# Optimization experiments

Measured on AMD Instinct MI355X. Metric: run time of the kernel, lower is better.

## Reference

```python
import jax, jax.numpy as jnp
import numpy as np

N, D, R, C_IN = 384, 256, 64, 2
REL_H, NEI_H = 128, 256


def setup_inputs() -> dict:
    key = jax.random.key(0)
    ks = jax.random.split(key, 16)
    inp = {
        "corr_index": jax.random.normal(ks[0], (N, N, C_IN), jnp.float32),
        "nei_index": jax.random.randint(ks[1], (N, N), 0, 2, jnp.int32),
        "nei_num": jax.random.randint(ks[2], (N,), 0, N, jnp.int32),
        "outgate": jax.random.uniform(ks[3], (N, D), jnp.float32),
        "self_h": jax.random.normal(ks[4], (N, D), jnp.float32),
        "self_c": jax.random.normal(ks[5], (N, D), jnp.float32),
        # relativeLayer: 2-layer MLP, relu after both layers (iflastac=True)
        "rel_w1": jax.random.normal(ks[6], (C_IN, REL_H), jnp.float32) * 0.1,
        "rel_b1": jnp.zeros((REL_H,), jnp.float32),
        "rel_w2": jax.random.normal(ks[7], (REL_H, R), jnp.float32) * 0.1,
        "rel_b2": jnp.zeros((R,), jnp.float32),
        # ngate: single Linear(R+2D -> D) + sigmoid
        "ngate_w": jax.random.normal(ks[8], (R + 2 * D, D), jnp.float32) * 0.005,
        "ngate_b": jnp.zeros((D,), jnp.float32),
        # WAr: single Linear(R+2D -> 1), no activation (WAr_ac='')
        "war_w": jax.random.normal(ks[9], (R + 2 * D, 1), jnp.float32) * 0.05,
        "war_b": jnp.zeros((1,), jnp.float32),
        # W_nei: Linear(D->NEI_H)+relu, Linear(NEI_H->D), no last activation
        "wnei_w1": jax.random.normal(ks[10], (D, NEI_H), jnp.float32) * 0.05,
        "wnei_b1": jnp.zeros((NEI_H,), jnp.float32),
        "wnei_w2": jax.random.normal(ks[11], (NEI_H, D), jnp.float32) * 0.05,
        "wnei_b2": jnp.zeros((D,), jnp.float32),
    }
    return inp


def reference(corr_index, nei_index, nei_num, outgate, self_h, self_c,
              rel_w1, rel_b1, rel_w2, rel_b2, ngate_w, ngate_b,
              war_w, war_b, wnei_w1, wnei_b1, wnei_w2, wnei_b2):
    n, d = self_h.shape
    mask = nei_index > 0  # [N, N], pair (i, j)
    # relativeLayer on pairwise relative coords: relu(relu(x W1 + b1) W2 + b2)
    r = jax.nn.relu(jax.nn.relu(corr_index @ rel_w1 + rel_b1) @ rel_w2 + rel_b2)  # [N,N,R]
    # In torch code flat index k = i*N + j: hi_t[k] = self_h[i], nei_inputs[k] = self_h[j]
    h_i = jnp.broadcast_to(self_h[:, None, :], (n, n, d))
    h_j = jnp.broadcast_to(self_h[None, :, :], (n, n, d))
    feat = jnp.concatenate([r, h_i, h_j], axis=-1)  # [N,N,R+2D]
    gate = jax.nn.sigmoid(feat @ ngate_w + ngate_b)  # [N,N,D]
    msg = h_j * gate
    tt = (feat @ war_w + war_b)[..., 0]  # [N,N] attention logits
    # scatter into zero-init matrix, then Pos[Pos==0] = -inf, row softmax
    pos = jnp.where(mask, tt, 0.0)
    pos = jnp.where(pos == 0.0, -jnp.inf, pos)
    pos = jax.nn.softmax(pos, axis=1)  # [N,N]
    # masked, attention-weighted messages; guard NaN from fully-masked rows
    H = jnp.where(mask[:, :, None], msg * pos[:, :, None], 0.0)  # [N,N,D]
    h_sum = jnp.sum(H, axis=1)  # [N,D]
    h_sum = jax.nn.relu(h_sum @ wnei_w1 + wnei_b1) @ wnei_w2 + wnei_b2
    C = h_sum + self_c
    H_out = outgate * jnp.tanh(C)
    return (outgate, H_out, C)
```

## Files before the change

kernel.cpp:

```cpp
#include <hip/hip_runtime.h>
#include <hip/hip_bf16.h>
#include <math.h>

#define N 384
#define D 256
#define R 64
#define RELH 128
#define NN (N*N)
#define ND (N*D)
#define JCHUNK 64
#define NCHUNK (N / JCHUNK)
#define TPB 16
#define LOG2E 1.44269504088896f
#define HS_STRIDE 264

typedef _Float16 f16x8 __attribute__((ext_vector_type(8)));
typedef _Float16 f16x2 __attribute__((ext_vector_type(2)));
typedef float f32x4 __attribute__((ext_vector_type(4)));

__device__ __forceinline__ float fast_sigmoid(float x) {
    float e = __builtin_amdgcn_exp2f(-LOG2E * x);
    return __builtin_amdgcn_rcpf(1.f + e);
}
__device__ __forceinline__ float fast_exp(float x) {
    return __builtin_amdgcn_exp2f(LOG2E * x);
}
__device__ __forceinline__ float fast_tanh(float x) {
    float e = __builtin_amdgcn_exp2f(2.f * LOG2E * x);
    return 1.f - 2.f * __builtin_amdgcn_rcpf(1.f + e);
}

__global__ __launch_bounds__(256) void prep_kernel(
        const float* __restrict__ self_h, const float* __restrict__ ngate_w,
        const float* __restrict__ ngate_b, const float* __restrict__ war_w,
        const float* __restrict__ wnei_w1, const float* __restrict__ wnei_w2,
        const float* __restrict__ rel_w2,
        float* __restrict__ A, float* __restrict__ Bm,
        unsigned int* __restrict__ bh,
        float* __restrict__ u, float* __restrict__ v,
        _Float16* __restrict__ wf,
        _Float16* __restrict__ wf1, _Float16* __restrict__ wf2,
        _Float16* __restrict__ wfr) {
    int b = blockIdx.x, tid = threadIdx.x;
    int wv = tid >> 6, l = tid & 63;
    int lg = l >> 4, ln = l & 15;

    if (b < 6) {
        int r0 = b * 64 + wv * 16;
        for (int rr = 0; rr < 16; ++rr) {
            int row = r0 + rr;
            float su = 0.f, sv = 0.f;
            #pragma unroll
            for (int k = 0; k < 4; ++k) {
                int d = k * 64 + l;
                float h = self_h[row * D + d];
                su = fmaf(h, war_w[R + d], su);
                sv = fmaf(h, war_w[R + D + d], sv);
            }
            #pragma unroll
            for (int off = 32; off; off >>= 1) {
                su += __shfl_down(su, off);
                sv += __shfl_down(sv, off);
            }
            if (l == 0) { u[row] = su; v[row] = sv; }
        }
    } else if (b < 54) {
        int W = (b - 6) * 4 + wv;
        int m0 = (W >> 3) * 16;
        int cb = (W & 7) * 64;
        const float* wsrc = ngate_w + (size_t)(cb >= 256 ? 320 : 64) * D + (cb & 255);
        f32x4 acc[4];
        #pragma unroll
        for (int nt = 0; nt < 4; ++nt) acc[nt] = (f32x4){0.f, 0.f, 0.f, 0.f};
        #pragma unroll
        for (int s = 0; s < 8; ++s) {
            const float4* hp = (const float4*)&self_h[(size_t)(m0 + ln) * D + s * 32 + lg * 8];
            float4 h0 = hp[0], h1 = hp[1];
            f16x8 af;
            af[0] = (_Float16)h0.x; af[1] = (_Float16)h0.y;
            af[2] = (_Float16)h0.z; af[3] = (_Float16)h0.w;
            af[4] = (_Float16)h1.x; af[5] = (_Float16)h1.y;
            af[6] = (_Float16)h1.z; af[7] = (_Float16)h1.w;
            #pragma unroll
            for (int nt = 0; nt < 4; ++nt) {
                f16x8 bf;
                #pragma unroll
                for (int ii = 0; ii < 8; ++ii)
                    bf[ii] = (_Float16)wsrc[(size_t)(s * 32 + lg * 8 + ii) * D + nt * 16 + ln];
                acc[nt] = __builtin_amdgcn_mfma_f32_16x16x32_f16(af, bf, acc[nt], 0, 0, 0);
            }
        }
        #pragma unroll
        for (int nt = 0; nt < 4; ++nt)
            #pragma unroll
            for (int reg = 0; reg < 4; ++reg) {
                int row = m0 + lg * 4 + reg;
                int col = cb + nt * 16 + ln;
                if (col < 256) {
                    A[row * D + col] = acc[nt][reg] + ngate_b[col];
                } else {
                    int c2 = col - 256;
                    float bmv = acc[nt][reg];
                    Bm[row * D + c2] = bmv;
                    f16x2 pk;
                    pk[0] = (_Float16)bmv;
                    pk[1] = (_Float16)self_h[row * D + c2];
                    bh[row * D + c2] = __builtin_bit_cast(unsigned int, pk);
                }
            }
    } else if (b < 62) {
        int blkEq = (b - 54) * 4 + wv;
        int s = blkEq >> 4, t = blkEq & 15;
        #pragma unroll
        for (int ii = 0; ii < 8; ++ii) {
            float w = ngate_w[(s * 32 + lg * 8 + ii) * D + t * 16 + ln];
            wf[((size_t)(s * 16 + t) * 64 + l) * 8 + ii] = (_Float16)w;
        }
    } else if (b < 78) {
        int base = ((b - 62) * 4 + wv) * 4;
        #pragma unroll
        for (int k = 0; k < 4; ++k) {
            int T = base + k;
            int mat = T >> 7, rem = T & 127;
            int s = rem >> 4, t = rem & 15;
            const float* wsrc = mat ? wnei_w2 : wnei_w1;
            _Float16* dst = mat ? wf2 : wf1;
            #pragma unroll
            for (int ii = 0; ii < 8; ++ii) {
                float w = wsrc[(size_t)(s * 32 + lg * 8 + ii) * D + t * 16 + ln];
                dst[((size_t)(s * 16 + t) * 64 + l) * 8 + ii] = (_Float16)w;
            }
        }
    } else {
        #pragma unroll
        for (int k = 0; k < 4; ++k) {
            int T = wv * 4 + k;
            int s = T >> 2, nt = T & 3;
            #pragma unroll
            for (int ii = 0; ii < 8; ++ii) {
                float w = rel_w2[(size_t)(s * 32 + lg * 8 + ii) * R + nt * 16 + ln];
                wfr[((size_t)(s * 4 + nt) * 64 + l) * 8 + ii] = (_Float16)w;
            }
        }
    }
}

__global__ __launch_bounds__(256) void fused_kernel(
        const float* __restrict__ corr,
        const float* __restrict__ rel_w1, const float* __restrict__ rel_b1,
        const float* __restrict__ rel_b2,
        const float* __restrict__ war_w, const float* __restrict__ v,
        const int* __restrict__ nei,
        const _Float16* __restrict__ wfr, const _Float16* __restrict__ wf,
        const float* __restrict__ A, const unsigned int* __restrict__ bh,
        float* __restrict__ hsum) {
    __shared__ __align__(16) _Float16 rlds[N * R];
    __shared__ float ttrow[N];
    __shared__ float red[4];
    __shared__ float sM, sS;
    int i = blockIdx.x, tid = threadIdx.x;
    int wv = tid >> 6, l = tid & 63;
    int lg = l >> 4, ln = l & 15;
    char* rbase = (char*)rlds;

    float w10[4][8], w11[4][8], b1v[4][8];
    #pragma unroll
    for (int s = 0; s < 4; ++s)
        #pragma unroll
        for (int ii = 0; ii < 8; ++ii) {
            int hk = s * 32 + lg * 8 + ii;
            w10[s][ii] = rel_w1[hk];
            w11[s][ii] = rel_w1[RELH + hk];
            b1v[s][ii] = rel_b1[hk];
        }
    float b2r[4], warw[4];
    #pragma unroll
    for (int nt = 0; nt < 4; ++nt) {
        b2r[nt]  = rel_b2[nt * 16 + ln];
        warw[nt] = war_w[nt * 16 + ln];
    }

    #pragma unroll
    for (int t = 0; t < 6; ++t) {
        int j0 = (wv * 6 + t) * 16;
        float2 x = ((const float2*)corr)[(size_t)i * N + j0 + ln];
        f16x8 af[4];
        #pragma unroll
        for (int s = 0; s < 4; ++s)
            #pragma unroll
            for (int ii = 0; ii < 8; ++ii) {
                float h = fmaxf(0.f, fmaf(x.y, w11[s][ii], fmaf(x.x, w10[s][ii], b1v[s][ii])));
                af[s][ii] = (_Float16)h;
            }
        f32x4 c[4];
        #pragma unroll
        for (int nt = 0; nt < 4; ++nt) c[nt] = (f32x4){0.f, 0.f, 0.f, 0.f};
        #pragma unroll
        for (int nt = 0; nt < 4; ++nt)
            #pragma unroll
            for (int s = 0; s < 4; ++s) {
                f16x8 bfv = *(const f16x8*)&wfr[((size_t)(s * 4 + nt) * 64 + l) * 8];
                c[nt] = __builtin_amdgcn_mfma_f32_16x16x32_f16(af[s], bfv, c[nt], 0, 0, 0);
            }
        float tpart[4] = {0.f, 0.f, 0.f, 0.f};
        #pragma unroll
        for (int nt = 0; nt < 4; ++nt)
            #pragma unroll
            for (int reg = 0; reg < 4; ++reg) {
                float rv = fmaxf(0.f, c[nt][reg] + b2r[nt]);
                int j = j0 + lg * 4 + reg;
                int off = (j * 128 + (nt * 16 + ln) * 2) ^ ((j & 7) << 4);
                *(_Float16*)(rbase + off) = (_Float16)rv;
                tpart[reg] = fmaf(rv, warw[nt], tpart[reg]);
            }
        #pragma unroll
        for (int reg = 0; reg < 4; ++reg) {
            float tsum = tpart[reg];
            #pragma unroll
            for (int off = 8; off; off >>= 1) tsum += __shfl_xor(tsum, off, 16);
            tpart[reg] = tsum;
        }
        if (ln == 0) {
            #pragma unroll
            for (int reg = 0; reg < 4; ++reg) {
                int j = j0 + lg * 4 + reg;
                ttrow[j] = tpart[reg] + v[j];
            }
        }
    }
    __syncthreads();

    {
        float tv1 = ttrow[tid];
        bool va1 = (nei[(size_t)i * N + tid] > 0) && (tv1 != 0.f);
        float tv2 = 0.f; bool va2 = false;
        if (tid < N - 256) {
            tv2 = ttrow[tid + 256];
            va2 = (nei[(size_t)i * N + tid + 256] > 0) && (tv2 != 0.f);
        }
        float m = va1 ? tv1 : -INFINITY;
        if (va2) m = fmaxf(m, tv2);
        #pragma unroll
        for (int off = 32; off; off >>= 1) m = fmaxf(m, __shfl_down(m, off));
        if (l == 0) red[wv] = m;
        __syncthreads();
        if (tid == 0) sM = fmaxf(fmaxf(red[0], red[1]), fmaxf(red[2], red[3]));
        __syncthreads();
        float M = sM;
        float e1 = 0.f, e2 = 0.f;
        if (M != -INFINITY) {
            if (va1) e1 = fast_exp(tv1 - M);
            if (va2) e2 = fast_exp(tv2 - M);
        }
        float sum = e1 + e2;
        #pragma unroll
        for (int off = 32; off; off >>= 1) sum += __shfl_down(sum, off);
        if (l == 0) red[wv] = sum;
        __syncthreads();
        if (tid == 0) sS = red[0] + red[1] + red[2] + red[3];
        __syncthreads();
        float rden = (sS > 0.f) ? __builtin_amdgcn_rcpf(sS) : 0.f;
        ttrow[tid] = va1 ? e1 * rden : 0.f;
        if (tid < N - 256) ttrow[tid + 256] = va2 ? e2 * rden : 0.f;
    }
    __syncthreads();

    f16x8 bf[2][4];
    #pragma unroll
    for (int s = 0; s < 2; ++s)
        #pragma unroll
        for (int dt = 0; dt < 4; ++dt)
            bf[s][dt] = *(const f16x8*)&wf[((size_t)(s * 16 + wv * 4 + dt) * 64 + l) * 8];
    float based[4];
    #pragma unroll
    for (int dt = 0; dt < 4; ++dt)
        based[dt] = A[i * D + wv * 64 + dt * 16 + ln];

    float acc[4] = {0.f, 0.f, 0.f, 0.f};
    for (int jt = 0; jt < 24; ++jt) {
        int jb = jt * 16;
        f16x8 afr[2];
        #pragma unroll
        for (int s = 0; s < 2; ++s) {
            int j = jb + ln;
            int off = (j * 128 + (s * 64 + lg * 16)) ^ ((j & 7) << 4);
            afr[s] = *(const f16x8*)(rbase + off);
        }
        f32x4 c[4];
        #pragma unroll
        for (int dt = 0; dt < 4; ++dt) c[dt] = (f32x4){0.f, 0.f, 0.f, 0.f};
        #pragma unroll
        for (int dt = 0; dt < 4; ++dt)
            #pragma unroll
            for (int s = 0; s < 2; ++s)
                c[dt] = __builtin_amdgcn_mfma_f32_16x16x32_f16(afr[s], bf[s][dt], c[dt], 0, 0, 0);
        #pragma unroll
        for (int reg = 0; reg < 4; ++reg) {
            int jj = jb + lg * 4 + reg;
            float p = ttrow[jj];
            #pragma unroll
            for (int dt = 0; dt < 4; ++dt) {
                int d = wv * 64 + dt * 16 + ln;
                unsigned int uu = bh[(size_t)jj * D + d];
                f16x2 bhv = __builtin_bit_cast(f16x2, uu);
                float logit = c[dt][reg] + based[dt] + (float)bhv[0];
                float g = fast_sigmoid(logit);
                acc[dt] = fmaf(p * g, (float)bhv[1], acc[dt]);
            }
        }
    }
    #pragma unroll
    for (int dt = 0; dt < 4; ++dt) {
        float a = acc[dt];
        a += __shfl_xor(a, 16);
        a += __shfl_xor(a, 32);
        acc[dt] = a;
    }
    if (lg == 0) {
        #pragma unroll
        for (int dt = 0; dt < 4; ++dt)
            hsum[(size_t)i * D + wv * 64 + dt * 16 + ln] = acc[dt];
    }
}

__global__ __launch_bounds__(256) void tt_valu_kernel(
        const float* __restrict__ corr,
        const float* __restrict__ rel_w1, const float* __restrict__ rel_b1,
        const float* __restrict__ rel_w2, const float* __restrict__ rel_b2,
        const float* __restrict__ war_w, const float* __restrict__ war_b,
        const float* __restrict__ u, const float* __restrict__ v,
        float* __restrict__ tt) {
    __shared__ __align__(16) float h1s[4][RELH];
    int tid = threadIdx.x, w = tid >> 6, l = tid & 63;
    float w1a0 = rel_w1[l],      w1a1 = rel_w1[RELH + l];
    float w1b0 = rel_w1[64 + l], w1b1 = rel_w1[RELH + 64 + l];
    float b1a = rel_b1[l], b1b = rel_b1[64 + l];
    float b2v = rel_b2[l], warw = war_w[l], wb = war_b[0];
    int pbase = blockIdx.x * TPB;
    #pragma unroll
    for (int it = 0; it < TPB / 4; ++it) {
        int p = pbase + it * 4 + w;
        int i = p / N, j = p - i * N;
        float2 x = *(const float2*)(corr + p * 2);
        h1s[w][l]      = fmaxf(0.f, fmaf(x.y, w1a1, fmaf(x.x, w1a0, b1a)));
        h1s[w][l + 64] = fmaxf(0.f, fmaf(x.y, w1b1, fmaf(x.x, w1b0, b1b)));
        float c0 = b2v, c1 = 0.f, c2 = 0.f, c3 = 0.f;
        const float4* hv = (const float4*)h1s[w];
        #pragma unroll
        for (int k4 = 0; k4 < RELH / 4; ++k4) {
            float4 h = hv[k4];
            c0 = fmaf(h.x, rel_w2[(k4 * 4 + 0) * R + l], c0);
            c1 = fmaf(h.y, rel_w2[(k4 * 4 + 1) * R + l], c1);
            c2 = fmaf(h.z, rel_w2[(k4 * 4 + 2) * R + l], c2);
            c3 = fmaf(h.w, rel_w2[(k4 * 4 + 3) * R + l], c3);
// ... 85 lines not shown
                c1 = fmaf(h.y, rel_w2[(k + 1) * R + l], c1);
                c2 = fmaf(h.z, rel_w2[(k + 2) * R + l], c2);
                c3 = fmaf(h.w, rel_w2[(k + 3) * R + l], c3);
            }
            rs[w][l] = fmaxf(0.f, (c0 + c1) + (c2 + c3));
        }
        __syncthreads();
        #pragma unroll
        for (int ww = 0; ww < 4; ++ww) {
            float wtj = wsh[ww];
            if (wtj != 0.f) {
                int jj = j0 + ww;
                const float4* rv = (const float4*)rs[ww];
                float l0 = 0.f, l1 = 0.f, l2 = 0.f, l3 = 0.f;
                #pragma unroll 4
                for (int m4 = 0; m4 < R / 4; ++m4) {
                    float4 r4 = rv[m4];
                    int m = m4 * 4;
                    l0 = fmaf(r4.x, ngate_w[m * D + tid], l0);
                    l1 = fmaf(r4.y, ngate_w[(m + 1) * D + tid], l1);
                    l2 = fmaf(r4.z, ngate_w[(m + 2) * D + tid], l2);
                    l3 = fmaf(r4.w, ngate_w[(m + 3) * D + tid], l3);
                }
                float logit = base + Bm[jj * D + tid] + ((l0 + l1) + (l2 + l3));
                float g = fast_sigmoid(logit);
                acc = fmaf(wtj * self_h[jj * D + tid], g, acc);
            }
        }
        __syncthreads();
    }
    partial[(blockIdx.y * N + i) * D + tid] = acc;
}

template<int CHUNKS>
__global__ __launch_bounds__(256, 2) void final_mfma_kernel(
        const float* __restrict__ partial,
        const _Float16* __restrict__ wf1, const _Float16* __restrict__ wf2,
        const float* __restrict__ wnei_b1, const float* __restrict__ wnei_b2,
        const float* __restrict__ self_c, const float* __restrict__ outgate,
        float* __restrict__ out) {
    __shared__ _Float16 hs16[16][HS_STRIDE];
    __shared__ _Float16 hid16[16][HS_STRIDE];
    int i0 = blockIdx.x * 16;
    int tid = threadIdx.x, wv = tid >> 6, l = tid & 63;
    int lg = l >> 4, ln = l & 15;

    #pragma unroll
    for (int s = 0; s < 4; ++s) {
        int f4 = tid + s * 256;
        int row = f4 >> 6, c4 = f4 & 63;
        float4 a = {0.f, 0.f, 0.f, 0.f};
        #pragma unroll
        for (int c = 0; c < CHUNKS; ++c) {
            float4 p = ((const float4*)partial)[(size_t)(c * N + i0 + row) * (D / 4) + c4];
            a.x += p.x; a.y += p.y; a.z += p.z; a.w += p.w;
        }
        hs16[row][c4 * 4 + 0] = (_Float16)a.x;
        hs16[row][c4 * 4 + 1] = (_Float16)a.y;
        hs16[row][c4 * 4 + 2] = (_Float16)a.z;
        hs16[row][c4 * 4 + 3] = (_Float16)a.w;
    }
    __syncthreads();

    {
        f32x4 c1[4];
        #pragma unroll
// ... 49 lines not shown
    }
}

extern "C" void kernel_launch(void* const* d_in, const int* in_sizes, int n_in,
                              void* d_out, int out_size, void* d_ws, size_t ws_size,
                              hipStream_t stream) {
    const float* corr    = (const float*)d_in[0];
    const int*   nei     = (const int*)d_in[1];
    const float* outg    = (const float*)d_in[3];
    const float* self_h  = (const float*)d_in[4];
    const float* self_c  = (const float*)d_in[5];
    const float* rel_w1  = (const float*)d_in[6];
    const float* rel_b1  = (const float*)d_in[7];
    const float* rel_w2  = (const float*)d_in[8];
    const float* rel_b2  = (const float*)d_in[9];
    const float* ngate_w = (const float*)d_in[10];
    const float* ngate_b = (const float*)d_in[11];
    const float* war_w   = (const float*)d_in[12];
    const float* war_b   = (const float*)d_in[13];
    const float* wnei_w1 = (const float*)d_in[14];
    const float* wnei_b1 = (const float*)d_in[15];
    const float* wnei_w2 = (const float*)d_in[16];
    const float* wnei_b2 = (const float*)d_in[17];

    float* ws      = (float*)d_ws;
    float* tt      = ws;
    float* pos     = ws + NN;
    float* A       = ws + 2 * NN;
    float* Bm      = ws + 2 * NN + ND;
    float* u       = ws + 2 * NN + 2 * ND;
    float* v       = u + N;
    float* partial = v + N;
    unsigned int* bh = (unsigned int*)(partial + NCHUNK * ND);
    float* tail    = (float*)(bh + ND);
    _Float16* wf   = (_Float16*)tail;
    _Float16* wf1  = wf + 2 * 16 * 64 * 8;
    _Float16* wf2  = wf1 + 8 * 16 * 64 * 8;
    _Float16* wfr  = wf2 + 8 * 16 * 64 * 8;
    size_t base_floats = (size_t)(2 * NN + 3 * ND + 2 * N + NCHUNK * ND);
    size_t f16_count = (size_t)(2 + 8 + 8) * 16 * 64 * 8 + 16 * 64 * 8;
    size_t need = (base_floats + f16_count / 2 + 16) * sizeof(float);
    bool use_fused = ws_size >= need;
    float* out = (float*)d_out;

    prep_kernel<<<79, 256, 0, stream>>>(self_h, ngate_w, ngate_b, war_w,
                                        wnei_w1, wnei_w2, rel_w2,
                                        A, Bm, bh, u, v, wf, wf1, wf2, wfr);
    if (use_fused) {
        fused_kernel<<<N, 256, 0, stream>>>(corr, rel_w1, rel_b1, rel_b2,
                                            war_w, v, nei, wfr, wf, A, bh, partial);
        final_mfma_kernel<1><<<N / 16, 256, 0, stream>>>(partial, wf1, wf2,
                                                         wnei_b1, wnei_b2,
                                                         self_c, outg, out);
    } else {
        tt_valu_kernel<<<NN / TPB, 256, 0, stream>>>(corr, rel_w1, rel_b1, rel_w2, rel_b2,
                                                     war_w, war_b, u, v, tt);
        softmax_kernel<<<N, 256, 0, stream>>>(tt, nei, pos);
        dim3 ggrid(N, NCHUNK);
        gate_norc_kernel<<<ggrid, 256, 0, stream>>>(corr, rel_w1, rel_b1, rel_w2, rel_b2,
                                                    ngate_w, A, Bm, pos, self_h,
                                                    partial);
        final_mfma_kernel<NCHUNK><<<N / 16, 256, 0, stream>>>(partial, wf1, wf2,
                                                              wnei_b1, wnei_b2,
                                                              self_c, outg, out);
    }
}
```

Measured before the change: 58.37 us.

## Split fused kernel over two j-halves per row and prefetch bh values

Launches the fused kernel on a 2D grid so each row i gets two blocks, each handling half of the neighbour columns for the gated message accumulation. The per-half results are written as partial sums that the final kernel reduces (template parameter now 2). LDS for the relative features is halved, which should allow more resident blocks. Each block still recomputes the full relative MLP and logits for the whole row so the softmax stays exact, so that stage's work is duplicated. It also hoists the bh loads ahead of the MFMA in each tile to hide their latency.

After: 66.52 us. 14.0% more time.

```diff
diff --git a/kernel.cpp b/kernel.cpp
--- a/kernel.cpp
+++ b/kernel.cpp
@@ -13,6 +13,7 @@
 #define TPB 16
 #define LOG2E 1.44269504088896f
 #define HS_STRIDE 264
+#define JH 192
 
 typedef _Float16 f16x8 __attribute__((ext_vector_type(8)));
 typedef _Float16 f16x2 __attribute__((ext_vector_type(2)));
@@ -153,78 +154,86 @@
         const int* __restrict__ nei,
         const _Float16* __restrict__ wfr, const _Float16* __restrict__ wf,
         const float* __restrict__ A, const unsigned int* __restrict__ bh,
-        float* __restrict__ hsum) {
-    __shared__ __align__(16) _Float16 rlds[N * R];
+        float* __restrict__ partial) {
+    __shared__ __align__(16) _Float16 rlds[JH * R];
     __shared__ float ttrow[N];
     __shared__ float red[4];
     __shared__ float sM, sS;
-    int i = blockIdx.x, tid = threadIdx.x;
+    int i = blockIdx.x, jhalf = blockIdx.y;
+    int jbase = jhalf * JH;
+    int tid = threadIdx.x;
     int wv = tid >> 6, l = tid & 63;
     int lg = l >> 4, ln = l & 15;
     char* rbase = (char*)rlds;
 
-    float w10[4][8], w11[4][8], b1v[4][8];
-    #pragma unroll
-    for (int s = 0; s < 4; ++s)
-        #pragma unroll
-        for (int ii = 0; ii < 8; ++ii) {
-            int hk = s * 32 + lg * 8 + ii;
-            w10[s][ii] = rel_w1[hk];
-            w11[s][ii] = rel_w1[RELH + hk];
-            b1v[s][ii] = rel_b1[hk];
-        }
-    float b2r[4], warw[4];
-    #pragma unroll
-    for (int nt = 0; nt < 4; ++nt) {
-        b2r[nt]  = rel_b2[nt * 16 + ln];
-        warw[nt] = war_w[nt * 16 + ln];
-    }
-
-    #pragma unroll
-    for (int t = 0; t < 6; ++t) {
-        int j0 = (wv * 6 + t) * 16;
-        float2 x = ((const float2*)corr)[(size_t)i * N + j0 + ln];
-        f16x8 af[4];
+    {
+        float w10[4][8], w11[4][8], b1v[4][8];
         #pragma unroll
         for (int s = 0; s < 4; ++s)
             #pragma unroll
             for (int ii = 0; ii < 8; ++ii) {
-                float h = fmaxf(0.f, fmaf(x.y, w11[s][ii], fmaf(x.x, w10[s][ii], b1v[s][ii])));
-                af[s][ii] = (_Float16)h;
-            }
-        f32x4 c[4];
-        #pragma unroll
-        for (int nt = 0; nt < 4; ++nt) c[nt] = (f32x4){0.f, 0.f, 0.f, 0.f};
-        #pragma unroll
-        for (int nt = 0; nt < 4; ++nt)
-            #pragma unroll
-            for (int s = 0; s < 4; ++s) {
-                f16x8 bfv = *(const f16x8*)&wfr[((size_t)(s * 4 + nt) * 64 + l) * 8];
-                c[nt] = __builtin_amdgcn_mfma_f32_16x16x32_f16(af[s], bfv, c[nt], 0, 0, 0);
-            }
-        float tpart[4] = {0.f, 0.f, 0.f, 0.f};
-        #pragma unroll
-        for (int nt = 0; nt < 4; ++nt)
+                int hk = s * 32 + lg * 8 + ii;
+                w10[s][ii] = rel_w1[hk];
+                w11[s][ii] = rel_w1[RELH + hk];
+                b1v[s][ii] = rel_b1[hk];
+            }
+        float b2r[4], warw[4];
+        #pragma unroll
+        for (int nt = 0; nt < 4; ++nt) {
+            b2r[nt]  = rel_b2[nt * 16 + ln];
+            warw[nt] = war_w[nt * 16 + ln];
+        }
+
+        #pragma unroll
+        for (int t = 0; t < 6; ++t) {
+            int tile = wv * 6 + t;
+            int j0 = tile * 16;
+            bool mine = (j0 >= jbase) && (j0 < jbase + JH);
+            float2 x = ((const float2*)corr)[(size_t)i * N + j0 + ln];
+            f16x8 af[4];
+            #pragma unroll
+            for (int s = 0; s < 4; ++s)
+                #pragma unroll
+                for (int ii = 0; ii < 8; ++ii) {
+                    float h = fmaxf(0.f, fmaf(x.y, w11[s][ii], fmaf(x.x, w10[s][ii], b1v[s][ii])));
+                    af[s][ii] = (_Float16)h;
+                }
+            f32x4 c[4];
+            #pragma unroll
+            for (int nt = 0; nt < 4; ++nt) c[nt] = (f32x4){0.f, 0.f, 0.f, 0.f};
+            #pragma unroll
+            for (int nt = 0; nt < 4; ++nt)
+                #pragma unroll
+                for (int s = 0; s < 4; ++s) {
+                    f16x8 bfv = *(const f16x8*)&wfr[((size_t)(s * 4 + nt) * 64 + l) * 8];
+                    c[nt] = __builtin_amdgcn_mfma_f32_16x16x32_f16(af[s], bfv, c[nt], 0, 0, 0);
+                }
+            float tpart[4] = {0.f, 0.f, 0.f, 0.f};
+            #pragma unroll
+            for (int nt = 0; nt < 4; ++nt)
+                #pragma unroll
+                for (int reg = 0; reg < 4; ++reg) {
+                    float rv = fmaxf(0.f, c[nt][reg] + b2r[nt]);
+                    if (mine) {
+                        int lj = j0 - jbase + lg * 4 + reg;
+                        int off = (lj * 128 + (nt * 16 + ln) * 2) ^ ((lj & 7) << 4);
+                        *(_Float16*)(rbase + off) = (_Float16)rv;
+                    }
+                    tpart[reg] = fmaf(rv, warw[nt], tpart[reg]);
+                }
             #pragma unroll
             for (int reg = 0; reg < 4; ++reg) {
-                float rv = fmaxf(0.f, c[nt][reg] + b2r[nt]);
-                int j = j0 + lg * 4 + reg;
-                int off = (j * 128 + (nt * 16 + ln) * 2) ^ ((j & 7) << 4);
-                *(_Float16*)(rbase + off) = (_Float16)rv;
-                tpart[reg] = fmaf(rv, warw[nt], tpart[reg]);
-            }
-        #pragma unroll
-        for (int reg = 0; reg < 4; ++reg) {
-            float tsum = tpart[reg];
-            #pragma unroll
-            for (int off = 8; off; off >>= 1) tsum += __shfl_xor(tsum, off, 16);
-            tpart[reg] = tsum;
-        }
-        if (ln == 0) {
-            #pragma unroll
-            for (int reg = 0; reg < 4; ++reg) {
-                int j = j0 + lg * 4 + reg;
-                ttrow[j] = tpart[reg] + v[j];
+                float tsum = tpart[reg];
+                #pragma unroll
+                for (int off = 8; off; off >>= 1) tsum += __shfl_xor(tsum, off, 16);
+                tpart[reg] = tsum;
+            }
+            if (ln == 0) {
+                #pragma unroll
+                for (int reg = 0; reg < 4; ++reg) {
+                    int j = j0 + lg * 4 + reg;
+                    ttrow[j] = tpart[reg] + v[j];
+                }
             }
         }
     }
@@ -277,13 +286,21 @@
         based[dt] = A[i * D + wv * 64 + dt * 16 + ln];
 
     float acc[4] = {0.f, 0.f, 0.f, 0.f};
-    for (int jt = 0; jt < 24; ++jt) {
-        int jb = jt * 16;
+    for (int jt = 0; jt < JH / 16; ++jt) {
+        int ljb = jt * 16;
+        unsigned int uu[4][4];
+        #pragma unroll
+        for (int reg = 0; reg < 4; ++reg) {
+            int jj = jbase + ljb + lg * 4 + reg;
+            #pragma unroll
+            for (int dt = 0; dt < 4; ++dt)
+                uu[reg][dt] = bh[(size_t)jj * D + wv * 64 + dt * 16 + ln];
+        }
         f16x8 afr[2];
         #pragma unroll
         for (int s = 0; s < 2; ++s) {
-            int j = jb + ln;
-            int off = (j * 128 + (s * 64 + lg * 16)) ^ ((j & 7) << 4);
+            int lj = ljb + ln;
+            int off = (lj * 128 + (s * 64 + lg * 16)) ^ ((lj & 7) << 4);
             afr[s] = *(const f16x8*)(rbase + off);
         }
         f32x4 c[4];
@@ -296,13 +313,11 @@
                 c[dt] = __builtin_amdgcn_mfma_f32_16x16x32_f16(afr[s], bf[s][dt], c[dt], 0, 0, 0);
         #pragma unroll
         for (int reg = 0; reg < 4; ++reg) {
-            int jj = jb + lg * 4 + reg;
+            int jj = jbase + ljb + lg * 4 + reg;
             float p = ttrow[jj];
             #pragma unroll
             for (int dt = 0; dt < 4; ++dt) {
-                int d = wv * 64 + dt * 16 + ln;
-                unsigned int uu = bh[(size_t)jj * D + d];
-                f16x2 bhv = __builtin_bit_cast(f16x2, uu);
+                f16x2 bhv = __builtin_bit_cast(f16x2, uu[reg][dt]);
                 float logit = c[dt][reg] + based[dt] + (float)bhv[0];
                 float g = fast_sigmoid(logit);
                 acc[dt] = fmaf(p * g, (float)bhv[1], acc[dt]);
@@ -319,7 +334,7 @@
     if (lg == 0) {
         #pragma unroll
         for (int dt = 0; dt < 4; ++dt)
-            hsum[(size_t)i * D + wv * 64 + dt * 16 + ln] = acc[dt];
+            partial[(size_t)(jhalf * N + i) * D + wv * 64 + dt * 16 + ln] = acc[dt];
     }
 }
 
@@ -601,9 +616,10 @@
                                         wnei_w1, wnei_w2, rel_w2,
                                         A, Bm, bh, u, v, wf, wf1, wf2, wfr);
     if (use_fused) {
-        fused_kernel<<<N, 256, 0, stream>>>(corr, rel_w1, rel_b1, rel_b2,
-                                            war_w, v, nei, wfr, wf, A, bh, partial);
-        final_mfma_kernel<1><<<N / 16, 256, 0, stream>>>(partial, wf1, wf2,
+        dim3 fgrid(N, 2);
+        fused_kernel<<<fgrid, 256, 0, stream>>>(corr, rel_w1, rel_b1, rel_b2,
+                                                war_w, v, nei, wfr, wf, A, bh, partial);
+        final_mfma_kernel<2><<<N / 16, 256, 0, stream>>>(partial, wf1, wf2,
                                                          wnei_b1, wnei_b2,
                                                          self_c, outg, out);
     } else {
```

## Prefetch gate operands, fold log2e into weights, pack layer-1 MLP in f16

Applied to the files above, without the earlier changes.

The gate loop in the fused kernel now double-buffers the bh global loads one tile ahead and seeds the MFMA accumulators with the per-row bias. The -log2e factor is folded into the prepared f16 ngate weights and the bh values, so the sigmoid becomes a bare exp2 plus reciprocal. The first relative-MLP layer is computed with packed f16x2 arithmetic instead of scalar fp32. The prep kernel is split into more, smaller tiles by raising its block count from 79 to 127. The goal is to hide global-load latency and cut VALU work. The cost is higher register pressure and lower precision in the first layer, which now runs in f16.

After: 66.09 us. 1.13x slower.

```diff
diff --git a/kernel.cpp b/kernel.cpp
--- a/kernel.cpp
+++ b/kernel.cpp
@@ -17,6 +17,8 @@
 typedef _Float16 f16x8 __attribute__((ext_vector_type(8)));
 typedef _Float16 f16x2 __attribute__((ext_vector_type(2)));
 typedef float f32x4 __attribute__((ext_vector_type(4)));
+
+union F16U8 { f16x8 v8; f16x2 p2[4]; };
 
 __device__ __forceinline__ float fast_sigmoid(float x) {
     float e = __builtin_amdgcn_exp2f(-LOG2E * x);
@@ -64,14 +66,14 @@
             }
             if (l == 0) { u[row] = su; v[row] = sv; }
         }
-    } else if (b < 54) {
+    } else if (b < 102) {
         int W = (b - 6) * 4 + wv;
-        int m0 = (W >> 3) * 16;
-        int cb = (W & 7) * 64;
+        int m0 = (W >> 4) * 16;
+        int cb = (W & 15) * 32;
         const float* wsrc = ngate_w + (size_t)(cb >= 256 ? 320 : 64) * D + (cb & 255);
-        f32x4 acc[4];
-        #pragma unroll
-        for (int nt = 0; nt < 4; ++nt) acc[nt] = (f32x4){0.f, 0.f, 0.f, 0.f};
+        f32x4 acc[2];
+        #pragma unroll
+        for (int nt = 0; nt < 2; ++nt) acc[nt] = (f32x4){0.f, 0.f, 0.f, 0.f};
         #pragma unroll
         for (int s = 0; s < 8; ++s) {
             const float4* hp = (const float4*)&self_h[(size_t)(m0 + ln) * D + s * 32 + lg * 8];
@@ -82,16 +84,16 @@
             af[4] = (_Float16)h1.x; af[5] = (_Float16)h1.y;
             af[6] = (_Float16)h1.z; af[7] = (_Float16)h1.w;
             #pragma unroll
-            for (int nt = 0; nt < 4; ++nt) {
+            for (int nt = 0; nt < 2; ++nt) {
                 f16x8 bf;
                 #pragma unroll
                 for (int ii = 0; ii < 8; ++ii)
-                    bf[ii] = (_Float16)wsrc[(size_t)(s * 32 + lg * 8 + ii) * D + nt * 16 + ln];
+                    bf[ii] = (_Float16)wsrc[(size_t)(s * 32 + lg * 8 + ii) * D + ((cb & 31) + nt * 16 + ln)];
                 acc[nt] = __builtin_amdgcn_mfma_f32_16x16x32_f16(af, bf, acc[nt], 0, 0, 0);
             }
         }
         #pragma unroll
-        for (int nt = 0; nt < 4; ++nt)
+        for (int nt = 0; nt < 2; ++nt)
             #pragma unroll
             for (int reg = 0; reg < 4; ++reg) {
                 int row = m0 + lg * 4 + reg;
@@ -103,21 +105,21 @@
                     float bmv = acc[nt][reg];
                     Bm[row * D + c2] = bmv;
                     f16x2 pk;
-                    pk[0] = (_Float16)bmv;
+                    pk[0] = (_Float16)(bmv * (-LOG2E));
                     pk[1] = (_Float16)self_h[row * D + c2];
                     bh[row * D + c2] = __builtin_bit_cast(unsigned int, pk);
                 }
             }
-    } else if (b < 62) {
-        int blkEq = (b - 54) * 4 + wv;
+    } else if (b < 110) {
+        int blkEq = (b - 102) * 4 + wv;
         int s = blkEq >> 4, t = blkEq & 15;
         #pragma unroll
         for (int ii = 0; ii < 8; ++ii) {
             float w = ngate_w[(s * 32 + lg * 8 + ii) * D + t * 16 + ln];
-            wf[((size_t)(s * 16 + t) * 64 + l) * 8 + ii] = (_Float16)w;
-        }
-    } else if (b < 78) {
-        int base = ((b - 62) * 4 + wv) * 4;
+            wf[((size_t)(s * 16 + t) * 64 + l) * 8 + ii] = (_Float16)(w * (-LOG2E));
+        }
+    } else if (b < 126) {
+        int base = ((b - 110) * 4 + wv) * 4;
         #pragma unroll
         for (int k = 0; k < 4; ++k) {
             int T = base + k;
@@ -163,68 +165,73 @@
     int lg = l >> 4, ln = l & 15;
     char* rbase = (char*)rlds;
 
-    float w10[4][8], w11[4][8], b1v[4][8];
-    #pragma unroll
-    for (int s = 0; s < 4; ++s)
-        #pragma unroll
-        for (int ii = 0; ii < 8; ++ii) {
-            int hk = s * 32 + lg * 8 + ii;
-            w10[s][ii] = rel_w1[hk];
-            w11[s][ii] = rel_w1[RELH + hk];
-            b1v[s][ii] = rel_b1[hk];
-        }
-    float b2r[4], warw[4];
-    #pragma unroll
-    for (int nt = 0; nt < 4; ++nt) {
-        b2r[nt]  = rel_b2[nt * 16 + ln];
-        warw[nt] = war_w[nt * 16 + ln];
-    }
-
-    #pragma unroll
-    for (int t = 0; t < 6; ++t) {
-        int j0 = (wv * 6 + t) * 16;
-        float2 x = ((const float2*)corr)[(size_t)i * N + j0 + ln];
-        f16x8 af[4];
+    {
+        f16x2 w10p[4][4], w11p[4][4], b1p[4][4];
         #pragma unroll
         for (int s = 0; s < 4; ++s)
             #pragma unroll
-            for (int ii = 0; ii < 8; ++ii) {
-                float h = fmaxf(0.f, fmaf(x.y, w11[s][ii], fmaf(x.x, w10[s][ii], b1v[s][ii])));
-                af[s][ii] = (_Float16)h;
-            }
-        f32x4 c[4];
-        #pragma unroll
-        for (int nt = 0; nt < 4; ++nt) c[nt] = (f32x4){0.f, 0.f, 0.f, 0.f};
-        #pragma unroll
-        for (int nt = 0; nt < 4; ++nt)
-            #pragma unroll
-            for (int s = 0; s < 4; ++s) {
-                f16x8 bfv = *(const f16x8*)&wfr[((size_t)(s * 4 + nt) * 64 + l) * 8];
-                c[nt] = __builtin_amdgcn_mfma_f32_16x16x32_f16(af[s], bfv, c[nt], 0, 0, 0);
-            }
-        float tpart[4] = {0.f, 0.f, 0.f, 0.f};
-        #pragma unroll
-        for (int nt = 0; nt < 4; ++nt)
+            for (int q = 0; q < 4; ++q) {
+                int hk = s * 32 + lg * 8 + q * 2;
+                w10p[s][q] = (f16x2){(_Float16)rel_w1[hk], (_Float16)rel_w1[hk + 1]};
+                w11p[s][q] = (f16x2){(_Float16)rel_w1[RELH + hk], (_Float16)rel_w1[RELH + hk + 1]};
+                b1p[s][q]  = (f16x2){(_Float16)rel_b1[hk], (_Float16)rel_b1[hk + 1]};
+            }
+        float b2r[4], warw[4];
+        #pragma unroll
+        for (int nt = 0; nt < 4; ++nt) {
+            b2r[nt]  = rel_b2[nt * 16 + ln];
+            warw[nt] = war_w[nt * 16 + ln];
+        }
+
+        #pragma unroll
+        for (int t = 0; t < 6; ++t) {
+            int j0 = (wv * 6 + t) * 16;
+            float2 x = ((const float2*)corr)[(size_t)i * N + j0 + ln];
+            _Float16 xh0 = (_Float16)x.x, xh1 = (_Float16)x.y;
+            f16x2 x0p = {xh0, xh0}, x1p = {xh1, xh1};
+            f16x2 zero2 = {(_Float16)0.f, (_Float16)0.f};
+            F16U8 af[4];
+            #pragma unroll
+            for (int s = 0; s < 4; ++s)
+                #pragma unroll
+                for (int q = 0; q < 4; ++q) {
+                    f16x2 hp = x0p * w10p[s][q] + (x1p * w11p[s][q] + b1p[s][q]);
+                    af[s].p2[q] = __builtin_elementwise_max(hp, zero2);
+                }
+            f32x4 c[4];
+            #pragma unroll
+            for (int nt = 0; nt < 4; ++nt) c[nt] = (f32x4){0.f, 0.f, 0.f, 0.f};
+            #pragma unroll
+            for (int nt = 0; nt < 4; ++nt)
+                #pragma unroll
+                for (int s = 0; s < 4; ++s) {
+                    f16x8 bfv = *(const f16x8*)&wfr[((size_t)(s * 4 + nt) * 64 + l) * 8];
+                    c[nt] = __builtin_amdgcn_mfma_f32_16x16x32_f16(af[s].v8, bfv, c[nt], 0, 0, 0);
+                }
+            float tpart[4] = {0.f, 0.f, 0.f, 0.f};
+            #pragma unroll
+            for (int nt = 0; nt < 4; ++nt)
+                #pragma unroll
+                for (int reg = 0; reg < 4; ++reg) {
+                    float rv = fmaxf(0.f, c[nt][reg] + b2r[nt]);
+                    int j = j0 + lg * 4 + reg;
+                    int off = (j * 128 + (nt * 16 + ln) * 2) ^ ((j & 7) << 4);
+                    *(_Float16*)(rbase + off) = (_Float16)rv;
+                    tpart[reg] = fmaf(rv, warw[nt], tpart[reg]);
+                }
             #pragma unroll
             for (int reg = 0; reg < 4; ++reg) {
-                float rv = fmaxf(0.f, c[nt][reg] + b2r[nt]);
-                int j = j0 + lg * 4 + reg;
-                int off = (j * 128 + (nt * 16 + ln) * 2) ^ ((j & 7) << 4);
-                *(_Float16*)(rbase + off) = (_Float16)rv;
-                tpart[reg] = fmaf(rv, warw[nt], tpart[reg]);
-            }
-        #pragma unroll
-        for (int reg = 0; reg < 4; ++reg) {
-            float tsum = tpart[reg];
-            #pragma unroll
-            for (int off = 8; off; off >>= 1) tsum += __shfl_xor(tsum, off, 16);
-            tpart[reg] = tsum;
-        }
-        if (ln == 0) {
-            #pragma unroll
-            for (int reg = 0; reg < 4; ++reg) {
-                int j = j0 + lg * 4 + reg;
-                ttrow[j] = tpart[reg] + v[j];
+                float tsum = tpart[reg];
+                #pragma unroll
+                for (int off = 8; off; off >>= 1) tsum += __shfl_xor(tsum, off, 16);
+                tpart[reg] = tsum;
+            }
+            if (ln == 0) {
+                #pragma unroll
+                for (int reg = 0; reg < 4; ++reg) {
+                    int j = j0 + lg * 4 + reg;
+                    ttrow[j] = tpart[reg] + v[j];
+                }
             }
         }
     }
@@ -274,41 +281,66 @@
     float based[4];
     #pragma unroll
     for (int dt = 0; dt < 4; ++dt)
-        based[dt] = A[i * D + wv * 64 + dt * 16 + ln];
+        based[dt] = (-LOG2E) * A[i * D + wv * 64 + dt * 16 + ln];
 
     float acc[4] = {0.f, 0.f, 0.f, 0.f};
-    for (int jt = 0; jt < 24; ++jt) {
-        int jb = jt * 16;
-        f16x8 afr[2];
-        #pragma unroll
-        for (int s = 0; s < 2; ++s) {
-            int j = jb + ln;
-            int off = (j * 128 + (s * 64 + lg * 16)) ^ ((j & 7) << 4);
-            afr[s] = *(const f16x8*)(rbase + off);
-        }
-        f32x4 c[4];
-        #pragma unroll
-        for (int dt = 0; dt < 4; ++dt) c[dt] = (f32x4){0.f, 0.f, 0.f, 0.f};
-        #pragma unroll
-        for (int dt = 0; dt < 4; ++dt)
-            #pragma unroll
-            for (int s = 0; s < 2; ++s)
-                c[dt] = __builtin_amdgcn_mfma_f32_16x16x32_f16(afr[s], bf[s][dt], c[dt], 0, 0, 0);
-        #pragma unroll
-        for (int reg = 0; reg < 4; ++reg) {
-            int jj = jb + lg * 4 + reg;
-            float p = ttrow[jj];
-            #pragma unroll
-            for (int dt = 0; dt < 4; ++dt) {
-                int d = wv * 64 + dt * 16 + ln;
-                unsigned int uu = bh[(size_t)jj * D + d];
-                f16x2 bhv = __builtin_bit_cast(f16x2, uu);
-                float logit = c[dt][reg] + based[dt] + (float)bhv[0];
-                float g = fast_sigmoid(logit);
-                acc[dt] = fmaf(p * g, (float)bhv[1], acc[dt]);
-            }
-        }
-    }
+
+    unsigned int uuA[4][4], uuB[4][4];
+    #define LOAD_UU(buf, jtv)                                                   \
+        {                                                                       \
+            int jb_ = (jtv) * 16;                                               \
+            _Pragma("unroll")                                                   \
+            for (int reg = 0; reg < 4; ++reg) {                                 \
+                int jj_ = jb_ + lg * 4 + reg;                                   \
+                _Pragma("unroll")                                               \
+                for (int dt = 0; dt < 4; ++dt)                                  \
+                    buf[reg][dt] = bh[(size_t)jj_ * D + wv * 64 + dt * 16 + ln];\
+            }                                                                   \
+        }
+    #define GATE_STEP(jtv, buf)                                                 \
+        {                                                                       \
+            int ljb_ = (jtv) * 16;                                              \
+            f16x8 afr[2];                                                       \
+            _Pragma("unroll")                                                   \
+            for (int s = 0; s < 2; ++s) {                                       \
+                int lj_ = ljb_ + ln;                                            \
+                int off_ = (lj_ * 128 + (s * 64 + lg * 16)) ^ ((lj_ & 7) << 4); \
+                afr[s] = *(const f16x8*)(rbase + off_);                         \
+            }                                                                   \
+            f32x4 c[4];                                                         \
+            _Pragma("unroll")                                                   \
+            for (int dt = 0; dt < 4; ++dt)                                      \
+                c[dt] = (f32x4){based[dt], based[dt], based[dt], based[dt]};    \
+            _Pragma("unroll")                                                   \
+            for (int dt = 0; dt < 4; ++dt)                                      \
+                _Pragma("unroll")                                               \
+                for (int s = 0; s < 2; ++s)                                     \
+                    c[dt] = __builtin_amdgcn_mfma_f32_16x16x32_f16(afr[s], bf[s][dt], c[dt], 0, 0, 0); \
+            _Pragma("unroll")                                                   \
+            for (int reg = 0; reg < 4; ++reg) {                                 \
+                int jj_ = ljb_ + lg * 4 + reg;                                  \
+                float p_ = ttrow[jj_];                                          \
+                _Pragma("unroll")                                               \
+                for (int dt = 0; dt < 4; ++dt) {                                \
+                    f16x2 bhv = __builtin_bit_cast(f16x2, buf[reg][dt]);        \
+                    float slog = c[dt][reg] + (float)bhv[0];                    \
+                    float g_ = __builtin_amdgcn_rcpf(1.f + __builtin_amdgcn_exp2f(slog)); \
+                    acc[dt] = fmaf(p_ * g_, (float)bhv[1], acc[dt]);            \
+                }                                                               \
+            }                                                                   \
+        }
+
+    LOAD_UU(uuA, 0);
+    #pragma unroll 2
+    for (int jt2 = 0; jt2 < 12; ++jt2) {
+        LOAD_UU(uuB, 2 * jt2 + 1);
+        GATE_STEP(2 * jt2, uuA);
+        if (jt2 < 11) LOAD_UU(uuA, 2 * jt2 + 2);
+        GATE_STEP(2 * jt2 + 1, uuB);
+    }
+    #undef LOAD_UU
+    #undef GATE_STEP
+
     #pragma unroll
     for (int dt = 0; dt < 4; ++dt) {
         float a = acc[dt];
@@ -597,9 +629,9 @@
     bool use_fused = ws_size >= need;
     float* out = (float*)d_out;
 
-    prep_kernel<<<79, 256, 0, stream>>>(self_h, ngate_w, ngate_b, war_w,
-                                        wnei_w1, wnei_w2, rel_w2,
-                                        A, Bm, bh, u, v, wf, wf1, wf2, wfr);
+    prep_kernel<<<127, 256, 0, stream>>>(self_h, ngate_w, ngate_b, war_w,
+                                         wnei_w1, wnei_w2, rel_w2,
+                                         A, Bm, bh, u, v, wf, wf1, wf2, wfr);
     if (use_fused) {
         fused_kernel<<<N, 256, 0, stream>>>(corr, rel_w1, rel_b1, rel_b2,
                                             war_w, v, nei, wfr, wf, A, bh, partial);
```

## Split fused kernel over j into three chunks with flash-style softmax merge

Applied to the files above, without the earlier changes.

The fused per-row kernel now runs on a 2D grid that splits the j dimension into three chunks, so there are three times as many blocks, each with a smaller LDS footprint. Each chunk computes a local max and sum of exponentials and writes them alongside unnormalised partial sums. A new final kernel rescales and combines the partials with online-softmax weights before the W_nei MLP. The aim is better occupancy and SM fill on a chip with many CUs, at the cost of extra partial traffic and a merge step. Chunks where 128 j values leave only two 16-row tiles per wave may give low per-block work.

After: 59.50 us. No clear change (+1.9%).

```diff
diff --git a/kernel.cpp b/kernel.cpp
--- a/kernel.cpp
+++ b/kernel.cpp
@@ -13,6 +13,8 @@
 #define TPB 16
 #define LOG2E 1.44269504088896f
 #define HS_STRIDE 264
+#define SPLIT 3
+#define JS (N / SPLIT)
 
 typedef _Float16 f16x8 __attribute__((ext_vector_type(8)));
 typedef _Float16 f16x2 __attribute__((ext_vector_type(2)));
@@ -153,93 +155,94 @@
         const int* __restrict__ nei,
         const _Float16* __restrict__ wfr, const _Float16* __restrict__ wf,
         const float* __restrict__ A, const unsigned int* __restrict__ bh,
-        float* __restrict__ hsum) {
-    __shared__ __align__(16) _Float16 rlds[N * R];
-    __shared__ float ttrow[N];
+        float* __restrict__ partial,
+        float* __restrict__ mbuf, float* __restrict__ sbuf) {
+    __shared__ __align__(16) _Float16 rlds[JS * R];
+    __shared__ float ttrow[JS];
     __shared__ float red[4];
     __shared__ float sM, sS;
-    int i = blockIdx.x, tid = threadIdx.x;
+    int i = blockIdx.x, chunk = blockIdx.y;
+    int jbase = chunk * JS;
+    int tid = threadIdx.x;
     int wv = tid >> 6, l = tid & 63;
     int lg = l >> 4, ln = l & 15;
     char* rbase = (char*)rlds;
 
-    float w10[4][8], w11[4][8], b1v[4][8];
-    #pragma unroll
-    for (int s = 0; s < 4; ++s)
-        #pragma unroll
-        for (int ii = 0; ii < 8; ++ii) {
-            int hk = s * 32 + lg * 8 + ii;
-            w10[s][ii] = rel_w1[hk];
-            w11[s][ii] = rel_w1[RELH + hk];
-            b1v[s][ii] = rel_b1[hk];
-        }
-    float b2r[4], warw[4];
-    #pragma unroll
-    for (int nt = 0; nt < 4; ++nt) {
-        b2r[nt]  = rel_b2[nt * 16 + ln];
-        warw[nt] = war_w[nt * 16 + ln];
-    }
-
-    #pragma unroll
-    for (int t = 0; t < 6; ++t) {
-        int j0 = (wv * 6 + t) * 16;
-        float2 x = ((const float2*)corr)[(size_t)i * N + j0 + ln];
-        f16x8 af[4];
+    {
+        float w10[4][8], w11[4][8], b1v[4][8];
         #pragma unroll
         for (int s = 0; s < 4; ++s)
             #pragma unroll
             for (int ii = 0; ii < 8; ++ii) {
-                float h = fmaxf(0.f, fmaf(x.y, w11[s][ii], fmaf(x.x, w10[s][ii], b1v[s][ii])));
-                af[s][ii] = (_Float16)h;
-            }
-        f32x4 c[4];
-        #pragma unroll
-        for (int nt = 0; nt < 4; ++nt) c[nt] = (f32x4){0.f, 0.f, 0.f, 0.f};
-        #pragma unroll
-        for (int nt = 0; nt < 4; ++nt)
-            #pragma unroll
-            for (int s = 0; s < 4; ++s) {
-                f16x8 bfv = *(const f16x8*)&wfr[((size_t)(s * 4 + nt) * 64 + l) * 8];
-                c[nt] = __builtin_amdgcn_mfma_f32_16x16x32_f16(af[s], bfv, c[nt], 0, 0, 0);
-            }
-        float tpart[4] = {0.f, 0.f, 0.f, 0.f};
-        #pragma unroll
-        for (int nt = 0; nt < 4; ++nt)
+                int hk = s * 32 + lg * 8 + ii;
+                w10[s][ii] = rel_w1[hk];
+                w11[s][ii] = rel_w1[RELH + hk];
+                b1v[s][ii] = rel_b1[hk];
+            }
+        float b2r[4], warw[4];
+        #pragma unroll
+        for (int nt = 0; nt < 4; ++nt) {
+            b2r[nt]  = rel_b2[nt * 16 + ln];
+            warw[nt] = war_w[nt * 16 + ln];
+        }
+
+        #pragma unroll
+        for (int t = 0; t < 2; ++t) {
+            int lj0 = (wv * 2 + t) * 16;
+            int jg0 = jbase + lj0;
+            float2 x = ((const float2*)corr)[(size_t)i * N + jg0 + ln];
+            f16x8 af[4];
+            #pragma unroll
+            for (int s = 0; s < 4; ++s)
+                #pragma unroll
+                for (int ii = 0; ii < 8; ++ii) {
+                    float h = fmaxf(0.f, fmaf(x.y, w11[s][ii], fmaf(x.x, w10[s][ii], b1v[s][ii])));
+                    af[s][ii] = (_Float16)h;
+                }
+            f32x4 c[4];
+            #pragma unroll
+            for (int nt = 0; nt < 4; ++nt) c[nt] = (f32x4){0.f, 0.f, 0.f, 0.f};
+            #pragma unroll
+            for (int nt = 0; nt < 4; ++nt)
+                #pragma unroll
+                for (int s = 0; s < 4; ++s) {
+                    f16x8 bfv = *(const f16x8*)&wfr[((size_t)(s * 4 + nt) * 64 + l) * 8];
+                    c[nt] = __builtin_amdgcn_mfma_f32_16x16x32_f16(af[s], bfv, c[nt], 0, 0, 0);
+                }
+            float tpart[4] = {0.f, 0.f, 0.f, 0.f};
+            #pragma unroll
+            for (int nt = 0; nt < 4; ++nt)
+                #pragma unroll
+                for (int reg = 0; reg < 4; ++reg) {
+                    float rv = fmaxf(0.f, c[nt][reg] + b2r[nt]);
+                    int lj = lj0 + lg * 4 + reg;
+                    int off = (lj * 128 + (nt * 16 + ln) * 2) ^ ((lj & 7) << 4);
+                    *(_Float16*)(rbase + off) = (_Float16)rv;
+                    tpart[reg] = fmaf(rv, warw[nt], tpart[reg]);
+                }
             #pragma unroll
             for (int reg = 0; reg < 4; ++reg) {
-                float rv = fmaxf(0.f, c[nt][reg] + b2r[nt]);
-                int j = j0 + lg * 4 + reg;
-                int off = (j * 128 + (nt * 16 + ln) * 2) ^ ((j & 7) << 4);
-                *(_Float16*)(rbase + off) = (_Float16)rv;
-                tpart[reg] = fmaf(rv, warw[nt], tpart[reg]);
-            }
-        #pragma unroll
-        for (int reg = 0; reg < 4; ++reg) {
-            float tsum = tpart[reg];
-            #pragma unroll
-            for (int off = 8; off; off >>= 1) tsum += __shfl_xor(tsum, off, 16);
-            tpart[reg] = tsum;
-        }
-        if (ln == 0) {
-            #pragma unroll
-            for (int reg = 0; reg < 4; ++reg) {
-                int j = j0 + lg * 4 + reg;
-                ttrow[j] = tpart[reg] + v[j];
+                float tsum = tpart[reg];
+                #pragma unroll
+                for (int off = 8; off; off >>= 1) tsum += __shfl_xor(tsum, off, 16);
+                tpart[reg] = tsum;
+            }
+            if (ln == 0) {
+                #pragma unroll
+                for (int reg = 0; reg < 4; ++reg) {
+                    int lj = lj0 + lg * 4 + reg;
+                    ttrow[lj] = tpart[reg] + v[jbase + lj];
+                }
             }
         }
     }
     __syncthreads();
 
     {
-        float tv1 = ttrow[tid];
-        bool va1 = (nei[(size_t)i * N + tid] > 0) && (tv1 != 0.f);
-        float tv2 = 0.f; bool va2 = false;
-        if (tid < N - 256) {
-            tv2 = ttrow[tid + 256];
-            va2 = (nei[(size_t)i * N + tid + 256] > 0) && (tv2 != 0.f);
-        }
-        float m = va1 ? tv1 : -INFINITY;
-        if (va2) m = fmaxf(m, tv2);
+        bool act = tid < JS;
+        float tv = act ? ttrow[tid] : 0.f;
+        bool va = act && (nei[(size_t)i * N + jbase + tid] > 0) && (tv != 0.f);
+        float m = va ? tv : -INFINITY;
         #pragma unroll
         for (int off = 32; off; off >>= 1) m = fmaxf(m, __shfl_down(m, off));
         if (l == 0) red[wv] = m;
@@ -247,21 +250,21 @@
         if (tid == 0) sM = fmaxf(fmaxf(red[0], red[1]), fmaxf(red[2], red[3]));
         __syncthreads();
         float M = sM;
-        float e1 = 0.f, e2 = 0.f;
-        if (M != -INFINITY) {
-            if (va1) e1 = fast_exp(tv1 - M);
-            if (va2) e2 = fast_exp(tv2 - M);
-        }
-        float sum = e1 + e2;
+        float e = 0.f;
+        if (va && M != -INFINITY) e = fast_exp(tv - M);
+        float sum = e;
         #pragma unroll
         for (int off = 32; off; off >>= 1) sum += __shfl_down(sum, off);
         if (l == 0) red[wv] = sum;
         __syncthreads();
-        if (tid == 0) sS = red[0] + red[1] + red[2] + red[3];
+        if (tid == 0) {
+            float ss = red[0] + red[1] + red[2] + red[3];
+            sS = ss;
+            mbuf[chunk * N + i] = M;
+            sbuf[chunk * N + i] = ss;
+        }
         __syncthreads();
-        float rden = (sS > 0.f) ? __builtin_amdgcn_rcpf(sS) : 0.f;
-        ttrow[tid] = va1 ? e1 * rden : 0.f;
-        if (tid < N - 256) ttrow[tid + 256] = va2 ? e2 * rden : 0.f;
+        if (act) ttrow[tid] = e;
     }
     __syncthreads();
 
@@ -277,13 +280,13 @@
         based[dt] = A[i * D + wv * 64 + dt * 16 + ln];
 
     float acc[4] = {0.f, 0.f, 0.f, 0.f};
-    for (int jt = 0; jt < 24; ++jt) {
+    for (int jt = 0; jt < JS / 16; ++jt) {
         int jb = jt * 16;
         f16x8 afr[2];
         #pragma unroll
         for (int s = 0; s < 2; ++s) {
-            int j = jb + ln;
-            int off = (j * 128 + (s * 64 + lg * 16)) ^ ((j & 7) << 4);
+            int lj = jb + ln;
+            int off = (lj * 128 + (s * 64 + lg * 16)) ^ ((lj & 7) << 4);
             afr[s] = *(const f16x8*)(rbase + off);
         }
         f32x4 c[4];
@@ -296,8 +299,9 @@
                 c[dt] = __builtin_amdgcn_mfma_f32_16x16x32_f16(afr[s], bf[s][dt], c[dt], 0, 0, 0);
         #pragma unroll
         for (int reg = 0; reg < 4; ++reg) {
-            int jj = jb + lg * 4 + reg;
-            float p = ttrow[jj];
+            int lj = jb + lg * 4 + reg;
+            float p = ttrow[lj];
+            int jj = jbase + lj;
             #pragma unroll
             for (int dt = 0; dt < 4; ++dt) {
                 int d = wv * 64 + dt * 16 + ln;
@@ -319,7 +323,7 @@
     if (lg == 0) {
         #pragma unroll
         for (int dt = 0; dt < 4; ++dt)
-            hsum[(size_t)i * D + wv * 64 + dt * 16 + ln] = acc[dt];
+            partial[(size_t)(chunk * N + i) * D + wv * 64 + dt * 16 + ln] = acc[dt];
     }
 }
 
@@ -471,6 +475,117 @@
     partial[(blockIdx.y * N + i) * D + tid] = acc;
 }
 
+__global__ __launch_bounds__(256, 2) void final_w_kernel(
+        const float* __restrict__ partial,
+        const float* __restrict__ mbuf, const float* __restrict__ sbuf,
+        const _Float16* __restrict__ wf1, const _Float16* __restrict__ wf2,
+        const float* __restrict__ wnei_b1, const float* __restrict__ wnei_b2,
+        const float* __restrict__ self_c, const float* __restrict__ outgate,
+        float* __restrict__ out) {
+    __shared__ _Float16 hs16[16][HS_STRIDE];
+    __shared__ _Float16 hid16[16][HS_STRIDE];
+    __shared__ float alpha[16][SPLIT];
+    int i0 = blockIdx.x * 16;
+    int tid = threadIdx.x, wv = tid >> 6, l = tid & 63;
+    int lg = l >> 4, ln = l & 15;
+
+    if (tid < 16) {
+        int row = i0 + tid;
+        float mv[SPLIT];
+        float M = -INFINITY;
+        #pragma unroll
+        for (int c = 0; c < SPLIT; ++c) {
+            mv[c] = mbuf[c * N + row];
+            M = fmaxf(M, mv[c]);
+        }
+        float a[SPLIT];
+        float S = 0.f;
+        #pragma unroll
+        for (int c = 0; c < SPLIT; ++c) {
+            float t = (mv[c] == -INFINITY) ? 0.f : fast_exp(mv[c] - M);
+            a[c] = t;
+            S = fmaf(t, sbuf[c * N + row], S);
+        }
+        float rden = (S > 0.f) ? __builtin_amdgcn_rcpf(S) : 0.f;
+        #pragma unroll
+        for (int c = 0; c < SPLIT; ++c) alpha[tid][c] = a[c] * rden;
+    }
+    __syncthreads();
+
+    #pragma unroll
+    for (int s = 0; s < 4; ++s) {
+        int f4 = tid + s * 256;
+        int row = f4 >> 6, c4 = f4 & 63;
+        float4 a = {0.f, 0.f, 0.f, 0.f};
+        #pragma unroll
+        for (int c = 0; c < SPLIT; ++c) {
+            float al = alpha[row][c];
+            float4 p = ((const float4*)partial)[(size_t)(c * N + i0 + row) * (D / 4) + c4];
+            a.x = fmaf(al, p.x, a.x); a.y = fmaf(al, p.y, a.y);
+            a.z = fmaf(al, p.z, a.z); a.w = fmaf(al, p.w, a.w);
+        }
+        hs16[row][c4 * 4 + 0] = (_Float16)a.x;
+        hs16[row][c4 * 4 + 1] = (_Float16)a.y;
+        hs16[row][c4 * 4 + 2] = (_Float16)a.z;
+        hs16[row][c4 * 4 + 3] = (_Float16)a.w;
+    }
+    __syncthreads();
+
+    {
+        f32x4 c1[4];
+        #pragma unroll
+        for (int dt = 0; dt < 4; ++dt) c1[dt] = (f32x4){0.f, 0.f, 0.f, 0.f};
+        #pragma unroll
+        for (int s = 0; s < 8; ++s) {
+            f16x8 a = *(const f16x8*)&hs16[ln][s * 32 + lg * 8];
+            #pragma unroll
+            for (int dt = 0; dt < 4; ++dt) {
+                f16x8 bfv = *(const f16x8*)&wf1[((size_t)(s * 16 + wv * 4 + dt) * 64 + l) * 8];
+                c1[dt] = __builtin_amdgcn_mfma_f32_16x16x32_f16(a, bfv, c1[dt], 0, 0, 0);
+            }
+        }
+        #pragma unroll
+        for (int dt = 0; dt < 4; ++dt) {
+            int col = wv * 64 + dt * 16 + ln;
+            float b1 = wnei_b1[col];
+            #pragma unroll
+            for (int reg = 0; reg < 4; ++reg)
+                hid16[lg * 4 + reg][col] = (_Float16)fmaxf(0.f, c1[dt][reg] + b1);
+        }
+    }
+    __syncthreads();
+
+    {
+        f32x4 c2[4];
+        #pragma unroll
+        for (int dt = 0; dt < 4; ++dt) c2[dt] = (f32x4){0.f, 0.f, 0.f, 0.f};
+        #pragma unroll
+        for (int s = 0; s < 8; ++s) {
+            f16x8 a = *(const f16x8*)&hid16[ln][s * 32 + lg * 8];
+            #pragma unroll
+            for (int dt = 0; dt < 4; ++dt) {
+                f16x8 bfv = *(const f16x8*)&wf2[((size_t)(s * 16 + wv * 4 + dt) * 64 + l) * 8];
+                c2[dt] = __builtin_amdgcn_mfma_f32_16x16x32_f16(a, bfv, c2[dt], 0, 0, 0);
+            }
+        }
+        #pragma unroll
+        for (int dt = 0; dt < 4; ++dt) {
+            int col = wv * 64 + dt * 16 + ln;
+            float b2 = wnei_b2[col];
+            #pragma unroll
+            for (int reg = 0; reg < 4; ++reg) {
+                int row = i0 + lg * 4 + reg;
+                int idx = row * D + col;
+                float C = c2[dt][reg] + b2 + self_c[idx];
+                float og = outgate[idx];
+                out[idx] = og;
+                out[ND + idx] = og * fast_tanh(C);
+                out[2 * ND + idx] = C;
+            }
+        }
+    }
+}
+
 template<int CHUNKS>
 __global__ __launch_bounds__(256, 2) void final_mfma_kernel(
         const float* __restrict__ partial,
@@ -586,12 +701,14 @@
     float* v       = u + N;
     float* partial = v + N;
     unsigned int* bh = (unsigned int*)(partial + NCHUNK * ND);
-    float* tail    = (float*)(bh + ND);
+    float* mbuf    = (float*)(bh + ND);
+    float* sbuf    = mbuf + SPLIT * N;
+    float* tail    = sbuf + SPLIT * N;
     _Float16* wf   = (_Float16*)tail;
     _Float16* wf1  = wf + 2 * 16 * 64 * 8;
     _Float16* wf2  = wf1 + 8 * 16 * 64 * 8;
     _Float16* wfr  = wf2 + 8 * 16 * 64 * 8;
-    size_t base_floats = (size_t)(2 * NN + 3 * ND + 2 * N + NCHUNK * ND);
+    size_t base_floats = (size_t)(2 * NN + 3 * ND + 2 * N + NCHUNK * ND + 2 * SPLIT * N);
     size_t f16_count = (size_t)(2 + 8 + 8) * 16 * 64 * 8 + 16 * 64 * 8;
     size_t need = (base_floats + f16_count / 2 + 16) * sizeof(float);
     bool use_fused = ws_size >= need;
@@ -601,11 +718,13 @@
                                         wnei_w1, wnei_w2, rel_w2,
                                         A, Bm, bh, u, v, wf, wf1, wf2, wfr);
     if (use_fused) {
-        fused_kernel<<<N, 256, 0, stream>>>(corr, rel_w1, rel_b1, rel_b2,
-                                            war_w, v, nei, wfr, wf, A, bh, partial);
-        final_mfma_kernel<1><<<N / 16, 256, 0, stream>>>(partial, wf1, wf2,
-                                                         wnei_b1, wnei_b2,
-                                                         self_c, outg, out);
+        dim3 fgrid(N, SPLIT);
+        fused_kernel<<<fgrid, 256, 0, stream>>>(corr, rel_w1, rel_b1, rel_b2,
+                                                war_w, v, nei, wfr, wf, A, bh,
+                                                partial, mbuf, sbuf);
+        final_w_kernel<<<N / 16, 256, 0, stream>>>(partial, mbuf, sbuf, wf1, wf2,
+                                                   wnei_b1, wnei_b2,
+                                                   self_c, outg, out);
     } else {
         tt_valu_kernel<<<NN / TPB, 256, 0, stream>>>(corr, rel_w1, rel_b1, rel_w2, rel_b2,
                                                      war_w, war_b, u, v, tt);
```
